# Performance work log

Hardware: AMD Instinct MI355X
Metric: run time of the kernel (lower is better)

Reference implementation:

```python
import jax, jax.numpy as jnp
import numpy as np

NUM_E = 1024        # codebook size
E_DIM = 256         # embedding dim (== channels of x)
BETA = 0.25

def setup_inputs() -> dict:
    key = jax.random.key(0)
    kx, kw = jax.random.split(key)
    x = jax.random.normal(kx, (16, E_DIM, 64, 64), dtype=jnp.float32)
    # embedding weight init: uniform(-1/num_e, 1/e_dim), matching torch init
    codebook = jax.random.uniform(kw, (NUM_E, E_DIM), dtype=jnp.float32,
                                  minval=-1.0 / NUM_E, maxval=1.0 / E_DIM)
    return {"x": x, "codebook": codebook}

def reference(x, codebook):
    beta = BETA
    # NCHW -> NHWC, flatten to [N, D]
    xp = jnp.transpose(x, (0, 2, 3, 1))          # [B,H,W,D]
    x_shape = xp.shape
    xf = xp.reshape(-1, E_DIM)                   # [N,D]
    cb_sq = jnp.sum(codebook ** 2, axis=1)                 # [K]
    in_sq = jnp.sum(xf ** 2, axis=1, keepdims=True)        # [N,1]
    dist = in_sq + cb_sq - 2.0 * (xf @ codebook.T)         # [N,K]
    idx = jnp.argmin(dist, axis=1)                         # [N]
    # one-hot encodings (returned like the torch module)
    encodings = jax.nn.one_hot(idx, NUM_E, dtype=jnp.float32)  # [N,K]
    # one-hot @ codebook == gather; use gather (same math, no big GEMM)
    xq = jnp.take(codebook, idx, axis=0).reshape(x_shape)      # [B,H,W,D]
    embedding_loss = jnp.mean((jax.lax.stop_gradient(xq) - xp) ** 2)
    quantization_loss = jnp.mean((xq - jax.lax.stop_gradient(xp)) ** 2)
    loss = quantization_loss + beta * embedding_loss
    e_mean = jnp.mean(encodings, axis=0)
    # NOTE: original code uses +1e10 inside the log (likely a typo for 1e-10);
    # we reproduce it faithfully.
    perplexity = jnp.exp(-jnp.sum(e_mean * jnp.log(e_mean + 10000000000.0)))
    # straight-through estimator
    xq_st = xp + jax.lax.stop_gradient(xq - xp)
    xq_out = jnp.transpose(xq_st, (0, 3, 1, 2))  # NHWC -> NCHW
    return (loss, xq_out, perplexity, encodings)
```

## Files before the change

kernel.cpp:

```cpp
#include <hip/hip_runtime.h>
#include <math.h>
#include <stdint.h>

typedef float f4u __attribute__((ext_vector_type(4), aligned(4)));
typedef __attribute__((ext_vector_type(8))) short short8;
typedef __attribute__((ext_vector_type(4))) float float4v;

#define DIM 256
#define KCB 1024
#define PERP_OFF 16777217
#define ENC_OFF  16777218
#define CAP 32
#define EPS 0.008f
#define NPB 128
#define MEGA_BLOCKS 512

__device__ __forceinline__ float np_sumsq128(const float* a, int stride) {
  float r[8];
  #pragma unroll
  for (int j = 0; j < 8; ++j) { float v = a[j * stride]; r[j] = __fmul_rn(v, v); }
  #pragma unroll
  for (int i = 8; i < 128; i += 8) {
    #pragma unroll
    for (int j = 0; j < 8; ++j) {
      float v = a[(i + j) * stride];
      r[j] = __fadd_rn(r[j], __fmul_rn(v, v));
    }
  }
  float s01 = __fadd_rn(r[0], r[1]);
  float s23 = __fadd_rn(r[2], r[3]);
  float s45 = __fadd_rn(r[4], r[5]);
  float s67 = __fadd_rn(r[6], r[7]);
  return __fadd_rn(__fadd_rn(s01, s23), __fadd_rn(s45, s67));
}

__device__ __forceinline__ unsigned short f2bf(float f) {
  unsigned u = __float_as_uint(f);
  u += 0x7FFFu + ((u >> 16) & 1u);
  return (unsigned short)(u >> 16);
}

__global__ __launch_bounds__(64)
void k_prep(const float* __restrict__ cb, unsigned short* __restrict__ e_bf16,
            float* __restrict__ cb_sq, int* __restrict__ counts) {
  const int k = blockIdx.x;
  const int l = threadIdx.x;
  float4 v = ((const float4*)(cb + k * DIM))[l];
  unsigned short bs[4] = {f2bf(v.x), f2bf(v.y), f2bf(v.z), f2bf(v.w)};
  *(ushort4*)(e_bf16 + k * DIM + l * 4) = *(ushort4*)bs;
  if (l == 0) {
    const float* p = cb + k * DIM;
    cb_sq[k] = __fadd_rn(np_sumsq128(p, 1), np_sumsq128(p + 128, 1));
    counts[k] = 0;
  }
}

__global__ __launch_bounds__(256, 3)
void k_mega(const float* __restrict__ x, const float* __restrict__ cb,
            const unsigned short* __restrict__ e_bf16,
            const float* __restrict__ cb_sq,
            float* __restrict__ out1, float* __restrict__ enc,
            int* __restrict__ counts, double* __restrict__ partials) {
  __shared__ unsigned int   lcnt[NPB];
  __shared__ unsigned short llist[NPB * CAP];
  __shared__ float          lsc[NPB * CAP];
  __shared__ float          lmin[NPB];
  __shared__ float          isq_s[NPB];
  __shared__ int            idxs[NPB];
  __shared__ double         sm[4];

  const int t    = threadIdx.x;
  const int wv   = t >> 6;
  const int lane = t & 63;
  const int l15  = lane & 15;
  const int quad = lane >> 4;
  const int blk  = blockIdx.x;
  if (t < NPB) lcnt[t] = 0;
  __syncthreads();

  short8 Bf[2][8];
  const int nbase = blk * NPB + wv * 32;
  #pragma unroll
  for (int g = 0; g < 2; ++g) {
    const int n = nbase + g * 16 + l15;
    const float* xb = x + (n >> 12) * 1048576 + (n & 4095);
    #pragma unroll
    for (int ks = 0; ks < 8; ++ks) {
      const int d0 = ks * 32 + quad * 8;
      union { unsigned short s[8]; short8 v; } u;
      #pragma unroll
      for (int j = 0; j < 8; ++j) u.s[j] = f2bf(xb[(d0 + j) * 4096]);
      Bf[g][ks] = u.v;
    }
  }

  float m[2] = {1e30f, 1e30f};
  for (int ct = 0; ct < 64; ++ct) {
    float4v acc[2];
    #pragma unroll
    for (int g = 0; g < 2; ++g) acc[g] = (float4v){0.f, 0.f, 0.f, 0.f};
    const unsigned short* ap = e_bf16 + (ct * 16 + l15) * DIM + quad * 8;
    #pragma unroll
    for (int ks = 0; ks < 8; ++ks) {
      const short8 a = *(const short8*)(ap + ks * 32);
      #pragma unroll
      for (int g = 0; g < 2; ++g)
        acc[g] = __builtin_amdgcn_mfma_f32_16x16x32_bf16(a, Bf[g][ks], acc[g], 0, 0, 0);
    }
    const float4 cs = *(const float4*)(cb_sq + ct * 16 + quad * 4);
    #pragma unroll
    for (int g = 0; g < 2; ++g) {
      const float sa[4] = {fmaf(-2.f, acc[g].x, cs.x), fmaf(-2.f, acc[g].y, cs.y),
                           fmaf(-2.f, acc[g].z, cs.z), fmaf(-2.f, acc[g].w, cs.w)};
      float bm = fminf(fminf(sa[0], sa[1]), fminf(sa[2], sa[3]));
      bm = fminf(bm, m[g]);
      bm = fminf(bm, __shfl_xor(bm, 16));
      bm = fminf(bm, __shfl_xor(bm, 32));
      m[g] = bm;
      const float thr = bm + EPS;
      const float sblk = fminf(fminf(sa[0], sa[1]), fminf(sa[2], sa[3]));
      if (sblk <= thr) {
        const int nl = wv * 32 + g * 16 + l15;
        #pragma unroll
        for (int r = 0; r < 4; ++r) {
          if (sa[r] <= thr) {
            unsigned slot = atomicAdd(&lcnt[nl], 1u);
            if (slot < CAP) {
              llist[nl * CAP + slot] = (unsigned short)(ct * 16 + quad * 4 + r);
              lsc[nl * CAP + slot]   = sa[r];
            }
          }
        }
      }
    }
  }
  if (quad == 0) {
    #pragma unroll
    for (int g = 0; g < 2; ++g) lmin[wv * 32 + g * 16 + l15] = m[g];
  }
  __syncthreads();

  if (t < NPB) {
    const unsigned cnt = lcnt[t];
    unsigned outc = cnt;
    if (cnt <= CAP) {
      const float thrf = lmin[t] + EPS;
      unsigned j = 0;
      for (unsigned i = 0; i < cnt; ++i) {
        const unsigned short c = llist[t * CAP + i];
        if (lsc[t * CAP + i] <= thrf) llist[t * CAP + j++] = c;
      }
      outc = j;
    }
    lcnt[t] = outc;
  } else {
    const int tt = t - NPB;
    const int n  = blk * NPB + tt;
    const float* p = x + (n >> 12) * 1048576 + (n & 4095);
    float h0 = np_sumsq128(p, 4096);
    float h1 = np_sumsq128(p + 128 * 4096, 4096);
    isq_s[tt] = __fadd_rn(h0, h1);
  }
  __syncthreads();

  {
    const int nl = t >> 1;
    const int q  = t & 1;
    const int n  = blk * NPB + nl;
    const unsigned cnt = lcnt[nl];
    const float* xb = x + (n >> 12) * 1048576 + (n & 4095);
    const float isq = isq_s[nl];
    float bv = 1e30f; int bc = 0x7FFFFFFF;

    if (cnt <= CAP) {
      const unsigned short* lst = llist + nl * CAP;
      for (unsigned i = q; i < cnt; i += 2) {
        const int c1 = lst[i];
        const float4* e1 = (const float4*)(cb + c1 * DIM);
        float d1 = 0.f;
        #pragma unroll 4
        for (int qq = 0; qq < 64; ++qq) {
          const float4 a = e1[qq];
          d1 = fmaf(xb[(qq * 4 + 0) * 4096], a.x, d1);
          d1 = fmaf(xb[(qq * 4 + 1) * 4096], a.y, d1);
          d1 = fmaf(xb[(qq * 4 + 2) * 4096], a.z, d1);
          d1 = fmaf(xb[(qq * 4 + 3) * 4096], a.w, d1);
        }
        const float dist = __fsub_rn(__fadd_rn(isq, cb_sq[c1]), __fmul_rn(2.f, d1));
        if (dist < bv || (dist == bv && c1 < bc)) { bv = dist; bc = c1; }
      }
    } else {
      for (int c = q; c < KCB; c += 2) {
        const float4* e1 = (const float4*)(cb + c * DIM);
        float d1 = 0.f;
        #pragma unroll 4
        for (int qq = 0; qq < 64; ++qq) {
          const float4 a = e1[qq];
          d1 = fmaf(xb[(qq * 4 + 0) * 4096], a.x, d1);
          d1 = fmaf(xb[(qq * 4 + 1) * 4096], a.y, d1);
          d1 = fmaf(xb[(qq * 4 + 2) * 4096], a.z, d1);
          d1 = fmaf(xb[(qq * 4 + 3) * 4096], a.w, d1);
        }
        const float dist = __fsub_rn(__fadd_rn(isq, cb_sq[c]), __fmul_rn(2.f, d1));
        if (dist < bv || (dist == bv && c < bc)) { bv = dist; bc = c; }
      }
    }
    {
      const float ov = __shfl_xor(bv, 1); const int oc = __shfl_xor(bc, 1);
      if (ov < bv || (ov == bv && oc < bc)) { bv = ov; bc = oc; }
    }
    if (q == 0) { idxs[nl] = bc; atomicAdd(counts + bc, 1); }
  }
  __syncthreads();

  const int w4 = (t & 15) * 4;
  const int cg = t >> 4;
  #pragma unroll
  for (int half = 0; half < 2; ++half) {
    const int bh = blk * 2 + half;
    const int b  = bh >> 6, h = bh & 63;
    const int* idx_h = idxs + half * 64;

    {
      float* base = enc + (size_t)bh * 65536 + t * 4;
      #pragma unroll 8
      for (int r = 0; r < 64; ++r) {
        const int bi = idx_h[r];
        f4u v = {0.f, 0.f, 0.f, 0.f};
        if ((bi >> 2) == t) {
          if ((bi & 3) == 0) v.x = 1.f; else if ((bi & 3) == 1) v.y = 1.f;
          else if ((bi & 3) == 2) v.z = 1.f; else v.w = 1.f;
        }
        __builtin_nontemporal_store(v, (f4u*)(base + r * 1024));
      }
    }

    float qf[4][16];
    #pragma unroll
    for (int i = 0; i < 4; ++i) {
      const float4* rp = (const float4*)(cb + idx_h[w4 + i] * DIM + cg * 16);
      #pragma unroll
      for (int jq = 0; jq < 4; ++jq) {
        const float4 v = rp[jq];
        qf[i][jq * 4 + 0] = v.x; qf[i][jq * 4 + 1] = v.y;
        qf[i][jq * 4 + 2] = v.z; qf[i][jq * 4 + 3] = v.w;
      }
    }

    double s = 0.0;
    #pragma unroll
    for (int j = 0; j < 16; ++j) {
      const int c = cg * 16 + j;
      const size_t off = ((size_t)b << 20) + ((size_t)c << 12) + (h << 6) + w4;
      const float4 xp = *(const float4*)(x + off);
      const float q0 = qf[0][j], q1 = qf[1][j], q2 = qf[2][j], q3 = qf[3][j];
      const float d0 = __fsub_rn(q0, xp.x), d1 = __fsub_rn(q1, xp.y);
      const float d2 = __fsub_rn(q2, xp.z), d3 = __fsub_rn(q3, xp.w);
      f4u o;
      o.x = __fadd_rn(xp.x, d0); o.y = __fadd_rn(xp.y, d1);
      o.z = __fadd_rn(xp.z, d2); o.w = __fadd_rn(xp.w, d3);
      __builtin_nontemporal_store(o, (f4u*)(out1 + off));
      s += (double)(d0*d0) + (double)(d1*d1) + (double)(d2*d2) + (double)(d3*d3);
    }
    #pragma unroll
    for (int off = 32; off > 0; off >>= 1) s += __shfl_down(s, off);
    if ((t & 63) == 0) sm[t >> 6] = s;
    __syncthreads();
    if (t == 0) partials[bh] = (sm[0] + sm[1]) + (sm[2] + sm[3]);
    __syncthreads();
  }
}

__global__ __launch_bounds__(256)
void k_final(const double* __restrict__ partials, const int* __restrict__ counts,
             float* __restrict__ out) {
  const int t = threadIdx.x;
  double s = 0.0;
  #pragma unroll
  for (int i = 0; i < 4; ++i) s += partials[t + i * 256];
  #pragma unroll
  for (int off = 32; off > 0; off >>= 1) s += __shfl_down(s, off);
  __shared__ double sm[4];
  __shared__ float smf[4];
  if ((t & 63) == 0) sm[t >> 6] = s;

  float ps = 0.f;
  #pragma unroll
  for (int i = 0; i < 4; ++i) {
    const float p = (float)counts[t + i * 256] * (1.0f / 65536.0f);
    ps += p * logf(1.0e10f + p);
  }
  #pragma unroll
  for (int off = 32; off > 0; off >>= 1) ps += __shfl_down(ps, off);
  if ((t & 63) == 0) smf[t >> 6] = ps;
  __syncthreads();
  if (t == 0) {
    const double tot = (sm[0] + sm[1]) + (sm[2] + sm[3]);
    const float mval = (float)(tot / 16777216.0);
    out[0] = mval + 0.25f * mval;
    out[PERP_OFF] = expf(-((smf[0] + smf[1]) + (smf[2] + smf[3])));
  }
}

extern "C" void kernel_launch(void* const* d_in, const int* in_sizes, int n_in,
                              void* d_out, int out_size, void* d_ws, size_t ws_size,
                              hipStream_t stream) {
  const float* x  = (const float*)d_in[0];
  const float* cb = (const float*)d_in[1];
  float* out = (float*)d_out;
  char*  ws  = (char*)d_ws;

  int*            counts   = (int*)(ws + 0);
  float*          cb_sq    = (float*)(ws + 4096);
  double*         partials = (double*)(ws + 8192);
  unsigned short* e_bf16   = (unsigned short*)(ws + 16384);

  k_prep <<<1024, 64, 0, stream>>>(cb, e_bf16, cb_sq, counts);
  k_mega <<<MEGA_BLOCKS, 256, 0, stream>>>(x, cb, e_bf16, cb_sq, out + 1,
                                           out + ENC_OFF, counts, partials);
  k_final<<<1, 256, 0, stream>>>(partials, counts, out);
}
```

Before: 598.4 us.

## Halve points per block to double grid size and occupancy in mega kernel

Each block now handles 64 points (one image row) instead of 128, so the grid doubles to 1024 blocks and the launch bound asks for 6 blocks per CU instead of 3. Each wave keeps one MFMA B-fragment group instead of two. The row-norm work is split across two threads per point, and the exact rescoring uses four threads per point with an extra shuffle reduction. The aim is more parallelism and latency hiding. In exchange each wave gets less MFMA reuse of the codebook A-fragment loads, so the bf16 codebook is read from L2 twice as often in total.

```diff
diff --git a/kernel.cpp b/kernel.cpp
--- a/kernel.cpp
+++ b/kernel.cpp
@@ -12,8 +12,8 @@
 #define ENC_OFF  16777218
 #define CAP 32
 #define EPS 0.008f
-#define NPB 128
-#define MEGA_BLOCKS 512
+#define NPB 64
+#define MEGA_BLOCKS 1024
 
 __device__ __forceinline__ float np_sumsq128(const float* a, int stride) {
   float r[8];
@@ -55,7 +55,7 @@
   }
 }
 
-__global__ __launch_bounds__(256, 3)
+__global__ __launch_bounds__(256, 6)
 void k_mega(const float* __restrict__ x, const float* __restrict__ cb,
             const unsigned short* __restrict__ e_bf16,
             const float* __restrict__ cb_sq,
@@ -65,7 +65,7 @@
   __shared__ unsigned short llist[NPB * CAP];
   __shared__ float          lsc[NPB * CAP];
   __shared__ float          lmin[NPB];
-  __shared__ float          isq_s[NPB];
+  __shared__ float          hpart[2 * NPB];
   __shared__ int            idxs[NPB];
   __shared__ double         sm[4];
 
@@ -78,11 +78,9 @@
   if (t < NPB) lcnt[t] = 0;
   __syncthreads();
 
-  short8 Bf[2][8];
-  const int nbase = blk * NPB + wv * 32;
-  #pragma unroll
-  for (int g = 0; g < 2; ++g) {
-    const int n = nbase + g * 16 + l15;
+  short8 Bf[8];
+  {
+    const int n = blk * NPB + wv * 16 + l15;
     const float* xb = x + (n >> 12) * 1048576 + (n & 4095);
     #pragma unroll
     for (int ks = 0; ks < 8; ++ks) {
@@ -90,54 +88,44 @@
       union { unsigned short s[8]; short8 v; } u;
       #pragma unroll
       for (int j = 0; j < 8; ++j) u.s[j] = f2bf(xb[(d0 + j) * 4096]);
-      Bf[g][ks] = u.v;
-    }
-  }
-
-  float m[2] = {1e30f, 1e30f};
+      Bf[ks] = u.v;
+    }
+  }
+
+  float m = 1e30f;
   for (int ct = 0; ct < 64; ++ct) {
-    float4v acc[2];
-    #pragma unroll
-    for (int g = 0; g < 2; ++g) acc[g] = (float4v){0.f, 0.f, 0.f, 0.f};
+    float4v acc = (float4v){0.f, 0.f, 0.f, 0.f};
     const unsigned short* ap = e_bf16 + (ct * 16 + l15) * DIM + quad * 8;
     #pragma unroll
     for (int ks = 0; ks < 8; ++ks) {
       const short8 a = *(const short8*)(ap + ks * 32);
+      acc = __builtin_amdgcn_mfma_f32_16x16x32_bf16(a, Bf[ks], acc, 0, 0, 0);
+    }
+    const float4 cs = *(const float4*)(cb_sq + ct * 16 + quad * 4);
+    const float sa[4] = {fmaf(-2.f, acc.x, cs.x), fmaf(-2.f, acc.y, cs.y),
+                         fmaf(-2.f, acc.z, cs.z), fmaf(-2.f, acc.w, cs.w)};
+    float bm = fminf(fminf(sa[0], sa[1]), fminf(sa[2], sa[3]));
+    const float sblk = bm;
+    bm = fminf(bm, m);
+    bm = fminf(bm, __shfl_xor(bm, 16));
+    bm = fminf(bm, __shfl_xor(bm, 32));
+    m = bm;
+    const float thr = bm + EPS;
+    if (sblk <= thr) {
+      const int nl = wv * 16 + l15;
       #pragma unroll
-      for (int g = 0; g < 2; ++g)
-        acc[g] = __builtin_amdgcn_mfma_f32_16x16x32_bf16(a, Bf[g][ks], acc[g], 0, 0, 0);
-    }
-    const float4 cs = *(const float4*)(cb_sq + ct * 16 + quad * 4);
-    #pragma unroll
-    for (int g = 0; g < 2; ++g) {
-      const float sa[4] = {fmaf(-2.f, acc[g].x, cs.x), fmaf(-2.f, acc[g].y, cs.y),
-                           fmaf(-2.f, acc[g].z, cs.z), fmaf(-2.f, acc[g].w, cs.w)};
-      float bm = fminf(fminf(sa[0], sa[1]), fminf(sa[2], sa[3]));
-      bm = fminf(bm, m[g]);
-      bm = fminf(bm, __shfl_xor(bm, 16));
-      bm = fminf(bm, __shfl_xor(bm, 32));
-      m[g] = bm;
-      const float thr = bm + EPS;
-      const float sblk = fminf(fminf(sa[0], sa[1]), fminf(sa[2], sa[3]));
-      if (sblk <= thr) {
-        const int nl = wv * 32 + g * 16 + l15;
-        #pragma unroll
-        for (int r = 0; r < 4; ++r) {
-          if (sa[r] <= thr) {
-            unsigned slot = atomicAdd(&lcnt[nl], 1u);
-            if (slot < CAP) {
-              llist[nl * CAP + slot] = (unsigned short)(ct * 16 + quad * 4 + r);
-              lsc[nl * CAP + slot]   = sa[r];
-            }
+      for (int r = 0; r < 4; ++r) {
+        if (sa[r] <= thr) {
+          unsigned slot = atomicAdd(&lcnt[nl], 1u);
+          if (slot < CAP) {
+            llist[nl * CAP + slot] = (unsigned short)(ct * 16 + quad * 4 + r);
+            lsc[nl * CAP + slot]   = sa[r];
           }
         }
       }
     }
   }
-  if (quad == 0) {
-    #pragma unroll
-    for (int g = 0; g < 2; ++g) lmin[wv * 32 + g * 16 + l15] = m[g];
-  }
+  if (quad == 0) lmin[wv * 16 + l15] = m;
   __syncthreads();
 
   if (t < NPB) {
@@ -153,28 +141,28 @@
       outc = j;
     }
     lcnt[t] = outc;
-  } else {
-    const int tt = t - NPB;
-    const int n  = blk * NPB + tt;
-    const float* p = x + (n >> 12) * 1048576 + (n & 4095);
-    float h0 = np_sumsq128(p, 4096);
-    float h1 = np_sumsq128(p + 128 * 4096, 4096);
-    isq_s[tt] = __fadd_rn(h0, h1);
+  } else if (t < 64 + 2 * NPB) {
+    const int tt = t - 64;
+    const int nl = tt >> 1;
+    const int p  = tt & 1;
+    const int n  = blk * NPB + nl;
+    const float* xp = x + (n >> 12) * 1048576 + (n & 4095) + p * 128 * 4096;
+    hpart[tt] = np_sumsq128(xp, 4096);
   }
   __syncthreads();
 
   {
-    const int nl = t >> 1;
-    const int q  = t & 1;
+    const int nl = t >> 2;
+    const int q  = t & 3;
     const int n  = blk * NPB + nl;
     const unsigned cnt = lcnt[nl];
     const float* xb = x + (n >> 12) * 1048576 + (n & 4095);
-    const float isq = isq_s[nl];
+    const float isq = __fadd_rn(hpart[2 * nl], hpart[2 * nl + 1]);
     float bv = 1e30f; int bc = 0x7FFFFFFF;
 
     if (cnt <= CAP) {
       const unsigned short* lst = llist + nl * CAP;
-      for (unsigned i = q; i < cnt; i += 2) {
+      for (unsigned i = q; i < cnt; i += 4) {
         const int c1 = lst[i];
         const float4* e1 = (const float4*)(cb + c1 * DIM);
         float d1 = 0.f;
@@ -190,7 +178,7 @@
         if (dist < bv || (dist == bv && c1 < bc)) { bv = dist; bc = c1; }
       }
     } else {
-      for (int c = q; c < KCB; c += 2) {
+      for (int c = q; c < KCB; c += 4) {
         const float4* e1 = (const float4*)(cb + c * DIM);
         float d1 = 0.f;
         #pragma unroll 4
@@ -206,69 +194,65 @@
       }
     }
     {
-      const float ov = __shfl_xor(bv, 1); const int oc = __shfl_xor(bc, 1);
+      float ov = __shfl_xor(bv, 1); int oc = __shfl_xor(bc, 1);
       if (ov < bv || (ov == bv && oc < bc)) { bv = ov; bc = oc; }
+      ov = __shfl_xor(bv, 2); oc = __shfl_xor(bc, 2);
+      if (ov < bv || (ov == bv && oc < bc)) { bv = ov; bc = oc; }
     }
     if (q == 0) { idxs[nl] = bc; atomicAdd(counts + bc, 1); }
   }
   __syncthreads();
+
+  const int bh = blk;
+  const int b  = bh >> 6, h = bh & 63;
+  {
+    float* base = enc + (size_t)bh * 65536 + t * 4;
+    #pragma unroll 8
+    for (int r = 0; r < 64; ++r) {
+      const int bi = idxs[r];
+      f4u v = {0.f, 0.f, 0.f, 0.f};
+      if ((bi >> 2) == t) {
+        if ((bi & 3) == 0) v.x = 1.f; else if ((bi & 3) == 1) v.y = 1.f;
+        else if ((bi & 3) == 2) v.z = 1.f; else v.w = 1.f;
+      }
+      __builtin_nontemporal_store(v, (f4u*)(base + r * 1024));
+    }
+  }
 
   const int w4 = (t & 15) * 4;
   const int cg = t >> 4;
-  #pragma unroll
-  for (int half = 0; half < 2; ++half) {
-    const int bh = blk * 2 + half;
-    const int b  = bh >> 6, h = bh & 63;
-    const int* idx_h = idxs + half * 64;
-
-    {
-      float* base = enc + (size_t)bh * 65536 + t * 4;
-      #pragma unroll 8
-      for (int r = 0; r < 64; ++r) {
-        const int bi = idx_h[r];
-        f4u v = {0.f, 0.f, 0.f, 0.f};
-        if ((bi >> 2) == t) {
-          if ((bi & 3) == 0) v.x = 1.f; else if ((bi & 3) == 1) v.y = 1.f;
-          else if ((bi & 3) == 2) v.z = 1.f; else v.w = 1.f;
-        }
-        __builtin_nontemporal_store(v, (f4u*)(base + r * 1024));
-      }
-    }
-
-    float qf[4][16];
+  float qf[4][16];
+  #pragma unroll
+  for (int i = 0; i < 4; ++i) {
+    const float4* rp = (const float4*)(cb + idxs[w4 + i] * DIM + cg * 16);
     #pragma unroll
-    for (int i = 0; i < 4; ++i) {
-      const float4* rp = (const float4*)(cb + idx_h[w4 + i] * DIM + cg * 16);
-      #pragma unroll
-      for (int jq = 0; jq < 4; ++jq) {
-        const float4 v = rp[jq];
-        qf[i][jq * 4 + 0] = v.x; qf[i][jq * 4 + 1] = v.y;
-        qf[i][jq * 4 + 2] = v.z; qf[i][jq * 4 + 3] = v.w;
-      }
-    }
-
-    double s = 0.0;
-    #pragma unroll
-    for (int j = 0; j < 16; ++j) {
-      const int c = cg * 16 + j;
-      const size_t off = ((size_t)b << 20) + ((size_t)c << 12) + (h << 6) + w4;
-      const float4 xp = *(const float4*)(x + off);
-      const float q0 = qf[0][j], q1 = qf[1][j], q2 = qf[2][j], q3 = qf[3][j];
-      const float d0 = __fsub_rn(q0, xp.x), d1 = __fsub_rn(q1, xp.y);
-      const float d2 = __fsub_rn(q2, xp.z), d3 = __fsub_rn(q3, xp.w);
-      f4u o;
-      o.x = __fadd_rn(xp.x, d0); o.y = __fadd_rn(xp.y, d1);
-      o.z = __fadd_rn(xp.z, d2); o.w = __fadd_rn(xp.w, d3);
-      __builtin_nontemporal_store(o, (f4u*)(out1 + off));
-      s += (double)(d0*d0) + (double)(d1*d1) + (double)(d2*d2) + (double)(d3*d3);
-    }
-    #pragma unroll
-    for (int off = 32; off > 0; off >>= 1) s += __shfl_down(s, off);
-    if ((t & 63) == 0) sm[t >> 6] = s;
-    __syncthreads();
-    if (t == 0) partials[bh] = (sm[0] + sm[1]) + (sm[2] + sm[3]);
-    __syncthreads();
-  }
+    for (int jq = 0; jq < 4; ++jq) {
+      const float4 v = rp[jq];
+      qf[i][jq * 4 + 0] = v.x; qf[i][jq * 4 + 1] = v.y;
+      qf[i][jq * 4 + 2] = v.z; qf[i][jq * 4 + 3] = v.w;
+    }
+  }
+
+  double s = 0.0;
+  #pragma unroll
+  for (int j = 0; j < 16; ++j) {
+    const int c = cg * 16 + j;
+    const size_t off = ((size_t)b << 20) + ((size_t)c << 12) + (h << 6) + w4;
+    const float4 xp = *(const float4*)(x + off);
+    const float q0 = qf[0][j], q1 = qf[1][j], q2 = qf[2][j], q3 = qf[3][j];
+    const float d0 = __fsub_rn(q0, xp.x), d1 = __fsub_rn(q1, xp.y);
+    const float d2 = __fsub_rn(q2, xp.z), d3 = __fsub_rn(q3, xp.w);
+    f4u o;
+    o.x = __fadd_rn(xp.x, d0); o.y = __fadd_rn(xp.y, d1);
+    o.z = __fadd_rn(xp.z, d2); o.w = __fadd_rn(xp.w, d3);
+    __builtin_nontemporal_store(o, (f4u*)(out1 + off));
+    s += (double)(d0*d0) + (double)(d1*d1) + (double)(d2*d2) + (double)(d3*d3);
+  }
+  #pragma unroll
+  for (int off = 32; off > 0; off >>= 1) s += __shfl_down(s, off);
+  if ((t & 63) == 0) sm[t >> 6] = s;
+  __syncthreads();
+  if (t == 0) partials[bh] = (sm[0] + sm[1]) + (sm[2] + sm[3]);
 }
 
 __global__ __launch_bounds__(256)
```

After: 699.0 us. +16.8%, slower.
